# Performance work log

Hardware: AMD Instinct MI355X
Metric: run time of the kernel (lower is better)

The kernel has to match this reference:

```python
import jax, jax.numpy as jnp
import numpy as np

B, S, DIM, H, DH = 2, 2048, 1024, 16, 64
EPS = 1e-6


def rms_norm(x, w):
    # x: (..., DH); computed in fp32 like the torch module
    norm = jax.lax.rsqrt(jnp.mean(jnp.square(x), axis=-1, keepdims=True) + EPS)
    return (x * norm) * w


def apply_rope(x, freqs):
    # x: (B, H, S, D), freqs: (S, D); torch code slices cos/sin to first half
    d = x.shape[-1] // 2
    cos = jnp.cos(freqs)[None, None, :, :d]
    sin = jnp.sin(freqs)[None, None, :, :d]
    x1, x2 = x[..., :d], x[..., d:]
    return jnp.concatenate([x1 * cos - x2 * sin, x2 * cos + x1 * sin], axis=-1)


def setup_inputs() -> dict:
    key = jax.random.key(0)
    ks = jax.random.split(key, 4)
    x = jax.random.normal(ks[0], (B, S, DIM), dtype=jnp.float32)
    # causal additive mask
    causal = jnp.tril(jnp.ones((S, S), dtype=bool))
    mask = jnp.where(causal, 0.0, -1e9).astype(jnp.float32)[None, None]
    # standard rope frequencies: pos * inv_freq over head_dim
    inv_freq = 1.0 / (10000.0 ** (jnp.arange(0, DH, dtype=jnp.float32) / DH))
    rope_freqs = jnp.arange(S, dtype=jnp.float32)[:, None] * inv_freq[None, :]
    total = H * DH
    w_qkv = jax.random.normal(ks[1], (3 * total, DIM), dtype=jnp.float32) * (DIM ** -0.5)
    w_out = jax.random.normal(ks[2], (DIM, total), dtype=jnp.float32) * (total ** -0.5)
    q_norm_w = jnp.ones((DH,), dtype=jnp.float32)
    k_norm_w = jnp.ones((DH,), dtype=jnp.float32)
    return {"x": x, "mask": mask, "rope_freqs": rope_freqs, "w_qkv": w_qkv,
            "w_out": w_out, "q_norm_w": q_norm_w, "k_norm_w": k_norm_w}


def reference(x, mask, rope_freqs, w_qkv, w_out, q_norm_w, k_norm_w):
    b, s, _ = x.shape
    qkv = (x @ w_qkv.T).reshape(b, s, 3, H, DH)
    q, k, v = qkv[:, :, 0], qkv[:, :, 1], qkv[:, :, 2]
    q = jnp.transpose(rms_norm(q, q_norm_w), (0, 2, 1, 3))  # (B,H,S,DH)
    k = jnp.transpose(rms_norm(k, k_norm_w), (0, 2, 1, 3))
    v = jnp.transpose(v, (0, 2, 1, 3))
    q = apply_rope(q, rope_freqs)
    k = apply_rope(k, rope_freqs)
    scale = DH ** -0.5
    attn = jnp.einsum('bhsd,bhtd->bhst', q, k) * scale + mask
    attn = jax.nn.softmax(attn, axis=-1)
    out = jnp.einsum('bhst,bhtd->bhsd', attn, v)
    out = jnp.transpose(out, (0, 2, 1, 3)).reshape(b, s, H * DH)
    return out @ w_out.T
```

## Files before the change

### kernel.cpp

```cpp
#include <hip/hip_runtime.h>
#include <hip/hip_bf16.h>
#include <stdint.h>

typedef short bf16x8 __attribute__((ext_vector_type(8)));
typedef float f32x4  __attribute__((ext_vector_type(4)));

#define MFMA_BF16(a,b,c) __builtin_amdgcn_mfma_f32_16x16x32_bf16((a),(b),(c),0,0,0)

__device__ __forceinline__ void async_ld16(const void* g, void* l) {
  __builtin_amdgcn_global_load_lds(
      (const __attribute__((address_space(1))) void*)g,
      (__attribute__((address_space(3))) void*)l, 16, 0, 0);
}

__device__ __forceinline__ unsigned short bf16_bits(float x) {
  __hip_bfloat16 h = __float2bfloat16(x);
  return *(unsigned short*)&h;
}

#define NX_C    (2 * 2048 * 1024)
#define NWQKV_C (3072 * 1024)
#define NWOUT_C (1024 * 1024)

__global__ void __launch_bounds__(256)
cvt_all(const float* __restrict__ x, const float* __restrict__ wqkv,
        const float* __restrict__ wout, __hip_bfloat16* __restrict__ dst)
{
  const int i = (blockIdx.x * 256 + threadIdx.x) * 4;
  const float* src;
  int off;
  if (i < NX_C)                { src = x;    off = i; }
  else if (i < NX_C + NWQKV_C) { src = wqkv; off = i - NX_C; }
  else                         { src = wout; off = i - NX_C - NWQKV_C; }
  const float4 v = *(const float4*)(src + off);
  ushort4 u;
  u.x = bf16_bits(v.x); u.y = bf16_bits(v.y);
  u.z = bf16_bits(v.z); u.w = bf16_bits(v.w);
  *(ushort4*)((unsigned short*)dst + i) = u;
}

template<int EPI>
__global__ void __launch_bounds__(256)
gemm_bt(const __hip_bfloat16* __restrict__ A,
        const __hip_bfloat16* __restrict__ B,
        int K,
        __hip_bfloat16* __restrict__ o0,
        __hip_bfloat16* __restrict__ o1,
        __hip_bfloat16* __restrict__ o2,
        float* __restrict__ of,
        const float* __restrict__ freqs,
        const float* __restrict__ qw,
        const float* __restrict__ kw)
{
  __shared__ __align__(16) __hip_bfloat16 As[2][2][128 * 32];
  __shared__ __align__(16) __hip_bfloat16 Bs[2][2][64 * 32];

  const int tid  = threadIdx.x;
  const int w    = tid >> 6;
  const int lane = tid & 63;
  const int quad = lane >> 4;
  const int l15  = lane & 15;

  const int m0 = blockIdx.y * 128;
  const int n0 = blockIdx.x * 64;

  const int srow = lane >> 2;
  const int sgr  = ((lane & 3) ^ ((lane >> 3) & 3)) * 8;
  const int c0 = w * 2, c1 = w * 2 + 1;

  const int pg = l15 * 32 + (quad ^ ((l15 >> 1) & 3)) * 8;

  const int wm  = w * 32;
  const int ac0 = w * 2;

  f32x4 acc[2][4] = {};

#define GSTAGE(KN, BUF) do {                                                        \
    _Pragma("unroll")                                                               \
    for (int s_ = 0; s_ < 2; ++s_) {                                                \
      async_ld16(A + (size_t)(m0 + c0 * 16 + srow) * K + (KN) + 32 * s_ + sgr,      \
                 &As[BUF][s_][0] + c0 * 512);                                       \
      async_ld16(A + (size_t)(m0 + c1 * 16 + srow) * K + (KN) + 32 * s_ + sgr,      \
                 &As[BUF][s_][0] + c1 * 512);                                       \
      async_ld16(B + (size_t)(n0 + w * 16 + srow) * K + (KN) + 32 * s_ + sgr,       \
                 &Bs[BUF][s_][0] + w * 512);                                        \
    }                                                                               \
  } while (0)

  const int niter = K >> 6;
  GSTAGE(0, 0);

  for (int it = 0; it < niter; ++it) {
    const int cur = it & 1;
    __syncthreads();
    if (it + 1 < niter) GSTAGE((it + 1) << 6, cur ^ 1);

#pragma unroll
    for (int s = 0; s < 2; ++s) {
      const __hip_bfloat16* Ac = &As[cur][s][0];
      const __hip_bfloat16* Bc = &Bs[cur][s][0];
      bf16x8 af[2], bfr[4];
      af[0] = *(const bf16x8*)(Ac + (ac0 + 0) * 512 + pg);
      af[1] = *(const bf16x8*)(Ac + (ac0 + 1) * 512 + pg);
#pragma unroll
      for (int t = 0; t < 4; ++t)
        bfr[t] = *(const bf16x8*)(Bc + t * 512 + pg);
#pragma unroll
      for (int mt = 0; mt < 2; ++mt)
#pragma unroll
        for (int nt = 0; nt < 4; ++nt)
          acc[mt][nt] = MFMA_BF16(af[mt], bfr[nt], acc[mt][nt]);
    }
  }
#undef GSTAGE

  if (EPI == 1) {
    const int ldc = (int)gridDim.x * 64;
#pragma unroll
    for (int mt = 0; mt < 2; ++mt)
#pragma unroll
      for (int nt = 0; nt < 4; ++nt)
#pragma unroll
        for (int r = 0; r < 4; ++r)
          of[(size_t)(m0 + wm + mt * 16 + quad * 4 + r) * ldc
             + n0 + nt * 16 + l15] = acc[mt][nt][r];
    return;
  }

  const int which = n0 >> 10;
  const int hb    = (n0 & 1023) >> 6;

  if (which == 2) {
#pragma unroll
    for (int mt = 0; mt < 2; ++mt)
#pragma unroll
      for (int nt = 0; nt < 4; ++nt)
#pragma unroll
        for (int r = 0; r < 4; ++r) {
          const int m = m0 + wm + mt * 16 + quad * 4 + r;
          const int b = m >> 11, s = m & 2047;
          const int d = nt * 16 + l15;
          o2[((size_t)((b * 16 + hb) * 64 + d) << 11) + s] =
              __float2bfloat16(acc[mt][nt][r]);
        }
    return;
  }

  const float* wgt = which ? kw : qw;
  __hip_bfloat16* dst = which ? o1 : o0;
  const float wv0 = wgt[l15], wv1 = wgt[16 + l15];
  const float wv2 = wgt[32 + l15], wv3 = wgt[48 + l15];

#pragma unroll
  for (int mt = 0; mt < 2; ++mt) {
#pragma unroll
    for (int r = 0; r < 4; ++r) {
      float ssq = acc[mt][0][r] * acc[mt][0][r] + acc[mt][1][r] * acc[mt][1][r]
                + acc[mt][2][r] * acc[mt][2][r] + acc[mt][3][r] * acc[mt][3][r];
      ssq += __shfl_xor(ssq, 1);
      ssq += __shfl_xor(ssq, 2);
      ssq += __shfl_xor(ssq, 4);
      ssq += __shfl_xor(ssq, 8);
      float sc = rsqrtf(ssq * (1.0f / 64.0f) + 1e-6f);
      if (which == 0) sc *= 0.125f;

      const float y0 = acc[mt][0][r] * sc * wv0;
      const float y1 = acc[mt][1][r] * sc * wv1;
      const float y2 = acc[mt][2][r] * sc * wv2;
      const float y3 = acc[mt][3][r] * sc * wv3;

      const int m = m0 + wm + mt * 16 + quad * 4 + r;
      const int b = m >> 11, s = m & 2047;
      const float f0 = freqs[s * 64 + l15];
      const float f1 = freqs[s * 64 + 16 + l15];
      float sn0, cs0, sn1, cs1;
      __sincosf(f0, &sn0, &cs0);
      __sincosf(f1, &sn1, &cs1);

      const size_t row = ((size_t)((b * 16 + hb) * 2048 + s)) << 6;
      dst[row + l15]      = __float2bfloat16(y0 * cs0 - y2 * sn0);
      dst[row + 16 + l15] = __float2bfloat16(y1 * cs1 - y3 * sn1);
      dst[row + 32 + l15] = __float2bfloat16(y2 * cs0 + y0 * sn0);
      dst[row + 48 + l15] = __float2bfloat16(y3 * cs1 + y1 * sn1);
    }
  }
}

__global__ void __launch_bounds__(256, 2)
attn(const __hip_bfloat16* __restrict__ q,
     const __hip_bfloat16* __restrict__ k,
     const __hip_bfloat16* __restrict__ vt,
     __hip_bfloat16* __restrict__ ao)
{
  __shared__ __align__(16) __hip_bfloat16 Ks[2][64 * 64];
  __shared__ __align__(16) __hip_bfloat16 Vs[2][64 * 64];

  const int tid  = threadIdx.x;
  const int w    = tid >> 6;
  const int lane = tid & 63;
  const int quad = lane >> 4;
  const int l15  = lane & 15;

  const int lin  = blockIdx.x;
  const int c8   = lin & 7;
  const int rest = lin >> 3;
  const int pj   = rest & 15;
  const int bh   = ((rest >> 4) << 3) + c8;
  const int b    = bh >> 4, h = bh & 15;

  const __hip_bfloat16* qb = q  + (size_t)bh * 2048 * 64;
  const __hip_bfloat16* kb = k  + (size_t)bh * 2048 * 64;
  const __hip_bfloat16* vb = vt + (size_t)bh * 64 * 2048;

  const int pr = ((l15 >> 2) * 8) + (l15 & 3);

  const int pgk  = (quad ^ (l15 & 3) ^ (((l15 >> 2) & 1) << 2)) * 8;
  const int pgk4 = pgk ^ 32;
  const int pgv  = (quad ^ (l15 & 7)) * 8;
  const int pgv4 = pgv ^ 32;

  const int sj  = lane >> 3;
  const int sp  = lane & 7;
  const int kgA = (sp ^ (sj & 3)) * 8;
  const int kgB = kgA ^ 32;
  const int vgs = (sp ^ sj) * 8;
  const int ck0 = w * 2, ck1 = w * 2 + 1;

#define STAGE(KEY0, BUF) do {                                                     \
    __hip_bfloat16* ks_ = &Ks[BUF][0];                                            \
    __hip_bfloat16* vs_ = &Vs[BUF][0];                                            \
    async_ld16(kb + (size_t)((KEY0) + ck0 * 8 + sj) * 64 + kgA, ks_ + ck0 * 512); \
    async_ld16(kb + (size_t)((KEY0) + ck1 * 8 + sj) * 64 + kgB, ks_ + ck1 * 512); \
    async_ld16(vb + (size_t)(ck0 * 8 + sj) * 2048 + (KEY0) + vgs, vs_ + ck0 * 512); \
    async_ld16(vb + (size_t)(ck1 * 8 + sj) * 2048 + (KEY0) + vgs, vs_ + ck1 * 512); \
  } while (0)

  for (int pass = 0; pass < 2; ++pass) {
    const int J  = pass ? (31 - pj) : pj;
    const int q0 = J * 64 + w * 16;
    const int qi = q0 + l15;

    const bf16x8 bq0 = *(const bf16x8*)(qb + (size_t)qi * 64 + quad * 8);
    const bf16x8 bq1 = *(const bf16x8*)(qb + (size_t)qi * 64 + 32 + quad * 8);

    f32x4 o[4] = {};
    float lsum = 0.f;

    const int ntile = J + 1;

    __syncthreads();
    STAGE(0, 0);

    for (int kt = 0; kt < ntile; ++kt) {
      const int cur = kt & 1;
      const int t0 = kt * 64;

      __syncthreads();
      if (kt + 1 < ntile) STAGE(t0 + 64, cur ^ 1);

      const __hip_bfloat16* Kc = &Ks[cur][0];
      const __hip_bfloat16* Vc = &Vs[cur][0];

      bf16x8 ka00, ka01, ka10, ka11, kb00, kb01, kb10, kb11;
      ka00 = *(const bf16x8*)(Kc + (pr)      * 64 + pgk);
      ka01 = *(const bf16x8*)(Kc + (pr)      * 64 + pgk4);
      ka10 = *(const bf16x8*)(Kc + (pr + 4)  * 64 + pgk);
      ka11 = *(const bf16x8*)(Kc + (pr + 4)  * 64 + pgk4);
      kb00 = *(const bf16x8*)(Kc + (32 + pr)     * 64 + pgk);
      kb01 = *(const bf16x8*)(Kc + (32 + pr)     * 64 + pgk4);
      kb10 = *(const bf16x8*)(Kc + (32 + pr + 4) * 64 + pgk);
      kb11 = *(const bf16x8*)(Kc + (32 + pr + 4) * 64 + pgk4);

      bf16x8 va[2][4];
#pragma unroll
      for (int dt = 0; dt < 4; ++dt) {
        va[0][dt] = *(const bf16x8*)(Vc + (dt * 16 + l15) * 64 + pgv);
        va[1][dt] = *(const bf16x8*)(Vc + (dt * 16 + l15) * 64 + pgv4);
      }

      f32x4 c00 = {}, c01 = {}, c10 = {}, c11 = {};
      c00 = MFMA_BF16(ka00, bq0, c00); c00 = MFMA_BF16(ka01, bq1, c00);
      c01 = MFMA_BF16(ka10, bq0, c01); c01 = MFMA_BF16(ka11, bq1, c01);
      c10 = MFMA_BF16(kb00, bq0, c10); c10 = MFMA_BF16(kb01, bq1, c10);
      c11 = MFMA_BF16(kb10, bq0, c11); c11 = MFMA_BF16(kb11, bq1, c11);

      float e00[4], e01[4], e10[4], e11[4];
#pragma unroll
      for (int r = 0; r < 4; ++r) {
        e00[r] = c00[r]; e01[r] = c01[r]; e10[r] = c10[r]; e11[r] = c11[r];
      }

      if (kt == ntile - 1) {
#pragma unroll
        for (int r = 0; r < 4; ++r) {
          const int k0v = t0 + 8 * quad + r;
          if (k0v      > qi) e00[r] = -1e30f;
          if (k0v + 4  > qi) e01[r] = -1e30f;
          if (k0v + 32 > qi) e10[r] = -1e30f;
          if (k0v + 36 > qi) e11[r] = -1e30f;
        }
      }

      float rs = 0.f;
#pragma unroll
      for (int r = 0; r < 4; ++r) {
        e00[r] = __expf(e00[r] - 8.0f);
        e01[r] = __expf(e01[r] - 8.0f);
        e10[r] = __expf(e10[r] - 8.0f);
        e11[r] = __expf(e11[r] - 8.0f);
        rs += (e00[r] + e01[r]) + (e10[r] + e11[r]);
      }
      lsum += rs;

      bf16x8 pf0, pf1;
#pragma unroll
      for (int r = 0; r < 4; ++r) {
        pf0[r] = (short)bf16_bits(e00[r]);  pf0[r + 4] = (short)bf16_bits(e01[r]);
        pf1[r] = (short)bf16_bits(e10[r]);  pf1[r + 4] = (short)bf16_bits(e11[r]);
      }

#pragma unroll
      for (int dt = 0; dt < 4; ++dt) {
        o[dt] = MFMA_BF16(va[0][dt], pf0, o[dt]);
        o[dt] = MFMA_BF16(va[1][dt], pf1, o[dt]);
      }
    }

    lsum += __shfl_xor(lsum, 16);
    lsum += __shfl_xor(lsum, 32);

    const float inv = 1.0f / lsum;
    const size_t row = ((size_t)(b * 2048 + qi)) * 1024 + h * 64;
#pragma unroll
    for (int dt = 0; dt < 4; ++dt) {
      ushort4 u;
      u.x = bf16_bits(o[dt][0] * inv);
      u.y = bf16_bits(o[dt][1] * inv);
      u.z = bf16_bits(o[dt][2] * inv);
      u.w = bf16_bits(o[dt][3] * inv);
      *(ushort4*)((unsigned short*)ao + row + dt * 16 + quad * 4) = u;
    }
  }
#undef STAGE
}

extern "C" void kernel_launch(void* const* d_in, const int* in_sizes, int n_in,
                              void* d_out, int out_size, void* d_ws, size_t ws_size,
                              hipStream_t stream)
{
  const float* x    = (const float*)d_in[0];
  const float* rf   = (const float*)d_in[2];
  const float* wqkv = (const float*)d_in[3];
  const float* wout = (const float*)d_in[4];
  const float* qw   = (const float*)d_in[5];
  const float* kw   = (const float*)d_in[6];

  const size_t NE = (size_t)2 * 16 * 2048 * 64;

  __hip_bfloat16* qb  = (__hip_bfloat16*)d_ws;
  __hip_bfloat16* kb  = qb  + NE;
  __hip_bfloat16* vt  = kb  + NE;
  __hip_bfloat16* ao  = vt  + NE;
  __hip_bfloat16* xb  = ao  + NE;
  __hip_bfloat16* wqb = xb  + NX_C;
  __hip_bfloat16* wob = wqb + NWQKV_C;

  cvt_all<<<(NX_C + NWQKV_C + NWOUT_C) / 1024, 256, 0, stream>>>(x, wqkv, wout, xb);

  gemm_bt<0><<<dim3(48, 32), 256, 0, stream>>>(xb, wqb, 1024, qb, kb, vt,
                                               nullptr, rf, qw, kw);
  attn<<<512, 256, 0, stream>>>(qb, kb, vt, ao);
  gemm_bt<1><<<dim3(16, 32), 256, 0, stream>>>(ao, wob, 1024,
                                               nullptr, nullptr, nullptr, (float*)d_out,
                                               nullptr, nullptr, nullptr);
}
```

Baseline: 190.6 us.

## Drop LDS staging in attention, load K/V directly per wave with 512-thread blocks

The attention kernel no longer stages K and V tiles through double-buffered shared memory with async global-to-LDS loads and barriers. Each wave now reads its MFMA operands straight from global memory. Blocks grow to 512 threads so the two causal query tiles (J and 31-J) run concurrently in separate waves rather than as two sequential passes. This removes barrier and LDS traffic, but each wave refetches K/V from global/L2 with no sharing across waves and uses uncoalesced strided loads. Waves in the same block also get uneven causal work.

Measured after the change: 272.2 us. 42.8% more time.

```diff
diff --git a/kernel.cpp b/kernel.cpp
--- a/kernel.cpp
+++ b/kernel.cpp
@@ -186,15 +186,12 @@
   }
 }
 
-__global__ void __launch_bounds__(256, 2)
+__global__ void __launch_bounds__(512)
 attn(const __hip_bfloat16* __restrict__ q,
      const __hip_bfloat16* __restrict__ k,
      const __hip_bfloat16* __restrict__ vt,
      __hip_bfloat16* __restrict__ ao)
 {
-  __shared__ __align__(16) __hip_bfloat16 Ks[2][64 * 64];
-  __shared__ __align__(16) __hip_bfloat16 Vs[2][64 * 64];
-
   const int tid  = threadIdx.x;
   const int w    = tid >> 6;
   const int lane = tid & 63;
@@ -214,134 +211,99 @@
 
   const int pr = ((l15 >> 2) * 8) + (l15 & 3);
 
-  const int pgk  = (quad ^ (l15 & 3) ^ (((l15 >> 2) & 1) << 2)) * 8;
-  const int pgk4 = pgk ^ 32;
-  const int pgv  = (quad ^ (l15 & 7)) * 8;
-  const int pgv4 = pgv ^ 32;
-
-  const int sj  = lane >> 3;
-  const int sp  = lane & 7;
-  const int kgA = (sp ^ (sj & 3)) * 8;
-  const int kgB = kgA ^ 32;
-  const int vgs = (sp ^ sj) * 8;
-  const int ck0 = w * 2, ck1 = w * 2 + 1;
-
-#define STAGE(KEY0, BUF) do {                                                     \
-    __hip_bfloat16* ks_ = &Ks[BUF][0];                                            \
-    __hip_bfloat16* vs_ = &Vs[BUF][0];                                            \
-    async_ld16(kb + (size_t)((KEY0) + ck0 * 8 + sj) * 64 + kgA, ks_ + ck0 * 512); \
-    async_ld16(kb + (size_t)((KEY0) + ck1 * 8 + sj) * 64 + kgB, ks_ + ck1 * 512); \
-    async_ld16(vb + (size_t)(ck0 * 8 + sj) * 2048 + (KEY0) + vgs, vs_ + ck0 * 512); \
-    async_ld16(vb + (size_t)(ck1 * 8 + sj) * 2048 + (KEY0) + vgs, vs_ + ck1 * 512); \
-  } while (0)
-
-  for (int pass = 0; pass < 2; ++pass) {
-    const int J  = pass ? (31 - pj) : pj;
-    const int q0 = J * 64 + w * 16;
-    const int qi = q0 + l15;
-
-    const bf16x8 bq0 = *(const bf16x8*)(qb + (size_t)qi * 64 + quad * 8);
-    const bf16x8 bq1 = *(const bf16x8*)(qb + (size_t)qi * 64 + 32 + quad * 8);
-
-    f32x4 o[4] = {};
-    float lsum = 0.f;
-
-    const int ntile = J + 1;
-
-    __syncthreads();
-    STAGE(0, 0);
-
-    for (int kt = 0; kt < ntile; ++kt) {
-      const int cur = kt & 1;
-      const int t0 = kt * 64;
-
-      __syncthreads();
-      if (kt + 1 < ntile) STAGE(t0 + 64, cur ^ 1);
-
-      const __hip_bfloat16* Kc = &Ks[cur][0];
-      const __hip_bfloat16* Vc = &Vs[cur][0];
-
-      bf16x8 ka00, ka01, ka10, ka11, kb00, kb01, kb10, kb11;
-      ka00 = *(const bf16x8*)(Kc + (pr)      * 64 + pgk);
-      ka01 = *(const bf16x8*)(Kc + (pr)      * 64 + pgk4);
-      ka10 = *(const bf16x8*)(Kc + (pr + 4)  * 64 + pgk);
-      ka11 = *(const bf16x8*)(Kc + (pr + 4)  * 64 + pgk4);
-      kb00 = *(const bf16x8*)(Kc + (32 + pr)     * 64 + pgk);
-      kb01 = *(const bf16x8*)(Kc + (32 + pr)     * 64 + pgk4);
-      kb10 = *(const bf16x8*)(Kc + (32 + pr + 4) * 64 + pgk);
-      kb11 = *(const bf16x8*)(Kc + (32 + pr + 4) * 64 + pgk4);
-
-      bf16x8 va[2][4];
-#pragma unroll
-      for (int dt = 0; dt < 4; ++dt) {
-        va[0][dt] = *(const bf16x8*)(Vc + (dt * 16 + l15) * 64 + pgv);
-        va[1][dt] = *(const bf16x8*)(Vc + (dt * 16 + l15) * 64 + pgv4);
+  const int J  = (w >> 2) ? (31 - pj) : pj;
+  const int qi = J * 64 + (w & 3) * 16 + l15;
+
+  const bf16x8 bq0 = *(const bf16x8*)(qb + (size_t)qi * 64 + quad * 8);
+  const bf16x8 bq1 = *(const bf16x8*)(qb + (size_t)qi * 64 + 32 + quad * 8);
+
+  f32x4 o[4] = {};
+  float lsum = 0.f;
+
+  for (int su = 0; su <= J; ++su) {
+    const int t0 = su * 64;
+    const bool diag = (su == J);
+
+    const __hip_bfloat16* kr = kb + (size_t)(t0 + pr) * 64 + quad * 8;
+    bf16x8 ka00 = *(const bf16x8*)(kr);
+    bf16x8 ka01 = *(const bf16x8*)(kr + 32);
+    bf16x8 ka10 = *(const bf16x8*)(kr + 4 * 64);
+    bf16x8 ka11 = *(const bf16x8*)(kr + 4 * 64 + 32);
+    bf16x8 kb00 = *(const bf16x8*)(kr + 32 * 64);
+    bf16x8 kb01 = *(const bf16x8*)(kr + 32 * 64 + 32);
+    bf16x8 kb10 = *(const bf16x8*)(kr + 36 * 64);
+    bf16x8 kb11 = *(const bf16x8*)(kr + 36 * 64 + 32);
+
+    bf16x8 va[2][4];
+#pragma unroll
+    for (int dt = 0; dt < 4; ++dt) {
+      const __hip_bfloat16* vr = vb + (size_t)(dt * 16 + l15) * 2048 + t0 + quad * 8;
+      va[0][dt] = *(const bf16x8*)(vr);
+      va[1][dt] = *(const bf16x8*)(vr + 32);
+    }
+
+    f32x4 c00 = {}, c01 = {}, c10 = {}, c11 = {};
+    c00 = MFMA_BF16(ka00, bq0, c00); c00 = MFMA_BF16(ka01, bq1, c00);
+    c01 = MFMA_BF16(ka10, bq0, c01); c01 = MFMA_BF16(ka11, bq1, c01);
+    c10 = MFMA_BF16(kb00, bq0, c10); c10 = MFMA_BF16(kb01, bq1, c10);
+    c11 = MFMA_BF16(kb10, bq0, c11); c11 = MFMA_BF16(kb11, bq1, c11);
+
+    float e00[4], e01[4], e10[4], e11[4];
+#pragma unroll
+    for (int r = 0; r < 4; ++r) {
+      e00[r] = c00[r]; e01[r] = c01[r]; e10[r] = c10[r]; e11[r] = c11[r];
+    }
+
+    if (diag) {
+#pragma unroll
+      for (int r = 0; r < 4; ++r) {
+        const int k0v = t0 + 8 * quad + r;
+        if (k0v      > qi) e00[r] = -1e30f;
+        if (k0v + 4  > qi) e01[r] = -1e30f;
+        if (k0v + 32 > qi) e10[r] = -1e30f;
+        if (k0v + 36 > qi) e11[r] = -1e30f;
       }
-
-      f32x4 c00 = {}, c01 = {}, c10 = {}, c11 = {};
-      c00 = MFMA_BF16(ka00, bq0, c00); c00 = MFMA_BF16(ka01, bq1, c00);
-      c01 = MFMA_BF16(ka10, bq0, c01); c01 = MFMA_BF16(ka11, bq1, c01);
-      c10 = MFMA_BF16(kb00, bq0, c10); c10 = MFMA_BF16(kb01, bq1, c10);
-      c11 = MFMA_BF16(kb10, bq0, c11); c11 = MFMA_BF16(kb11, bq1, c11);
-
-      float e00[4], e01[4], e10[4], e11[4];
-#pragma unroll
-      for (int r = 0; r < 4; ++r) {
-        e00[r] = c00[r]; e01[r] = c01[r]; e10[r] = c10[r]; e11[r] = c11[r];
-      }
-
-      if (kt == ntile - 1) {
-#pragma unroll
-        for (int r = 0; r < 4; ++r) {
-          const int k0v = t0 + 8 * quad + r;
-          if (k0v      > qi) e00[r] = -1e30f;
-          if (k0v + 4  > qi) e01[r] = -1e30f;
-          if (k0v + 32 > qi) e10[r] = -1e30f;
-          if (k0v + 36 > qi) e11[r] = -1e30f;
-        }
-      }
-
-      float rs = 0.f;
-#pragma unroll
-      for (int r = 0; r < 4; ++r) {
-        e00[r] = __expf(e00[r] - 8.0f);
-        e01[r] = __expf(e01[r] - 8.0f);
-        e10[r] = __expf(e10[r] - 8.0f);
-        e11[r] = __expf(e11[r] - 8.0f);
-        rs += (e00[r] + e01[r]) + (e10[r] + e11[r]);
-      }
-      lsum += rs;
-
-      bf16x8 pf0, pf1;
-#pragma unroll
-      for (int r = 0; r < 4; ++r) {
-        pf0[r] = (short)bf16_bits(e00[r]);  pf0[r + 4] = (short)bf16_bits(e01[r]);
-        pf1[r] = (short)bf16_bits(e10[r]);  pf1[r + 4] = (short)bf16_bits(e11[r]);
-      }
-
-#pragma unroll
-      for (int dt = 0; dt < 4; ++dt) {
-        o[dt] = MFMA_BF16(va[0][dt], pf0, o[dt]);
-        o[dt] = MFMA_BF16(va[1][dt], pf1, o[dt]);
-      }
-    }
-
-    lsum += __shfl_xor(lsum, 16);
-    lsum += __shfl_xor(lsum, 32);
-
-    const float inv = 1.0f / lsum;
-    const size_t row = ((size_t)(b * 2048 + qi)) * 1024 + h * 64;
+    }
+
+    float rs = 0.f;
+#pragma unroll
+    for (int r = 0; r < 4; ++r) {
+      e00[r] = __expf(e00[r] - 8.0f);
+      e01[r] = __expf(e01[r] - 8.0f);
+      e10[r] = __expf(e10[r] - 8.0f);
+      e11[r] = __expf(e11[r] - 8.0f);
+      rs += (e00[r] + e01[r]) + (e10[r] + e11[r]);
+    }
+    lsum += rs;
+
+    bf16x8 pf0, pf1;
+#pragma unroll
+    for (int r = 0; r < 4; ++r) {
+      pf0[r] = (short)bf16_bits(e00[r]);  pf0[r + 4] = (short)bf16_bits(e01[r]);
+      pf1[r] = (short)bf16_bits(e10[r]);  pf1[r + 4] = (short)bf16_bits(e11[r]);
+    }
+
 #pragma unroll
     for (int dt = 0; dt < 4; ++dt) {
-      ushort4 u;
-      u.x = bf16_bits(o[dt][0] * inv);
-      u.y = bf16_bits(o[dt][1] * inv);
-      u.z = bf16_bits(o[dt][2] * inv);
-      u.w = bf16_bits(o[dt][3] * inv);
-      *(ushort4*)((unsigned short*)ao + row + dt * 16 + quad * 4) = u;
-    }
-  }
-#undef STAGE
+      o[dt] = MFMA_BF16(va[0][dt], pf0, o[dt]);
+      o[dt] = MFMA_BF16(va[1][dt], pf1, o[dt]);
+    }
+  }
+
+  lsum += __shfl_xor(lsum, 16);
+  lsum += __shfl_xor(lsum, 32);
+
+  const float inv = 1.0f / lsum;
+  const size_t row = ((size_t)(b * 2048 + qi)) * 1024 + h * 64;
+#pragma unroll
+  for (int dt = 0; dt < 4; ++dt) {
+    ushort4 u;
+    u.x = bf16_bits(o[dt][0] * inv);
+    u.y = bf16_bits(o[dt][1] * inv);
+    u.z = bf16_bits(o[dt][2] * inv);
+    u.w = bf16_bits(o[dt][3] * inv);
+    *(ushort4*)((unsigned short*)ao + row + dt * 16 + quad * 4) = u;
+  }
 }
 
 extern "C" void kernel_launch(void* const* d_in, const int* in_sizes, int n_in,
@@ -369,7 +331,7 @@
 
   gemm_bt<0><<<dim3(48, 32), 256, 0, stream>>>(xb, wqb, 1024, qb, kb, vt,
                                                nullptr, rf, qw, kw);
-  attn<<<512, 256, 0, stream>>>(qb, kb, vt, ao);
+  attn<<<512, 512, 0, stream>>>(qb, kb, vt, ao);
   gemm_bt<1><<<dim3(16, 32), 256, 0, stream>>>(ao, wob, 1024,
                                                nullptr, nullptr, nullptr, (float*)d_out,
                                                nullptr, nullptr, nullptr);
```
